# Optimization experiments

Hardware: AMD Instinct MI355X
Metric: run time of the kernel (lower is better)

Reference implementation:

```python
import jax, jax.numpy as jnp
import numpy as np

B, T, F, U, L = 64, 512, 256, 1024, 3
LN_EPS = 1e-12  # tf.contrib.layers.layer_norm default


def setup_inputs() -> dict:
    key = jax.random.key(0)
    ks = jax.random.split(key, 8)

    def w(k, shape):
        return jax.random.normal(k, shape, jnp.float32) / np.float32(np.sqrt(shape[0]))

    return {
        "input": jax.random.normal(ks[0], (B, T, F), jnp.float32),
        "conditioned_lst": jax.random.randint(ks[1], (T,), 0, 2).astype(bool),
        # LSTM layer 0: input = feature F, layers 1..2: input = U
        "W0": w(ks[2], (F + U, 4 * U)), "b0": jnp.zeros((4 * U,), jnp.float32),
        "W1": w(ks[3], (2 * U, 4 * U)), "b1": jnp.zeros((4 * U,), jnp.float32),
        "W2": w(ks[4], (2 * U, 4 * U)), "b2": jnp.zeros((4 * U,), jnp.float32),
        # output dense projection back to feature dim
        "Wd": w(ks[5], (U, F)), "bd": jnp.zeros((F,), jnp.float32),
        # layer norm params
        "gamma": jnp.ones((F,), jnp.float32), "beta": jnp.zeros((F,), jnp.float32),
    }


def _lstm_cell(x, h, c, W, b):
    # BasicLSTMCell: gates in (i, j, f, o) order, forget_bias = 1.0
    z = jnp.dot(jnp.concatenate([x, h], axis=-1), W) + b
    i, j, f, o = jnp.split(z, 4, axis=-1)
    c_new = c * jax.nn.sigmoid(f + 1.0) + jax.nn.sigmoid(i) * jnp.tanh(j)
    h_new = jax.nn.sigmoid(o) * jnp.tanh(c_new)
    return h_new, c_new


def reference(input, conditioned_lst, W0, b0, W1, b1, W2, b2, Wd, bd, gamma, beta):
    Ws, bs = [W0, W1, W2], [b0, b1, b2]
    xs = (jnp.arange(T), jnp.swapaxes(input, 0, 1), conditioned_lst)  # time-major
    carry0 = (jnp.zeros((L, B, U), input.dtype),  # h per layer
              jnp.zeros((L, B, U), input.dtype),  # c per layer
              jnp.zeros((B, F), input.dtype))     # previous emit

    def step(carry, xt):
        hs, cs, prev_emit = carry
        t, x_t, cond_t = xt
        # auto-conditioning: teacher-force on conditioned steps (and step 0)
        x = jnp.where(jnp.logical_or(t == 0, cond_t), x_t, prev_emit)
        new_h, new_c = [], []
        for l in range(L):
            h, c = _lstm_cell(x, hs[l], cs[l], Ws[l], bs[l])
            new_h.append(h)
            new_c.append(c)
            x = h
        y = jnp.dot(x, Wd) + bd  # dense projection [B, F]
        mu = jnp.mean(y, axis=-1, keepdims=True)
        var = jnp.mean(jnp.square(y - mu), axis=-1, keepdims=True)
        y = (y - mu) * jax.lax.rsqrt(var + LN_EPS) * gamma + beta
        emit = jax.nn.relu(y)
        return (jnp.stack(new_h), jnp.stack(new_c), emit), emit

    _, outs = jax.lax.scan(step, carry0, xs)  # [T, B, F]
    return jnp.swapaxes(outs, 0, 1)  # [B, T, F]
```

## Files before the change

kernel.cpp:

```cpp
#include <hip/hip_runtime.h>
#include <math.h>

#define B 64
#define T 512
#define F 256
#define U 1024
#define NBLK 256
#define NTH 512
#define WPAD 68

typedef unsigned short ushort_t;
typedef __attribute__((ext_vector_type(8))) _Float16 f16x8_t;
typedef __attribute__((ext_vector_type(4))) float f32x4_t;

static const size_t OFF_STATS= 0;
static const size_t OFF_COND = 4096;
static const size_t OFF_BAR  = 6144;
static const size_t OFF_H2B  = 7424;
static const size_t OFF_HS   = 269568;
static const size_t OFF_YB   = 1056000;
static const size_t OFF_PW0  = 1088768;
static const size_t OFF_PW1  = 11574528;
static const size_t OFF_PW2  = 28351744;
static const size_t ZERO_BYTES = OFF_PW0;

__device__ __forceinline__ float sigm(float x) {
    return 1.0f / (1.0f + __expf(-x));
}

__device__ __forceinline__ ushort_t f2h(float x) {
    _Float16 h = (_Float16)x;
    union { _Float16 h; ushort_t u; } v; v.h = h;
    return v.u;
}
__device__ __forceinline__ float h2f(ushort_t u) {
    union { ushort_t u; _Float16 h; } v; v.u = u;
    return (float)v.h;
}

__device__ __forceinline__ void store_uc_b64(void* p, unsigned long long v) {
    asm volatile("global_store_dwordx2 %0, %1, off sc0 sc1"
                 :: "v"(p), "v"(v) : "memory");
}
__device__ __forceinline__ void store_uc_b128(void* p, f32x4_t v) {
    asm volatile("global_store_dwordx4 %0, %1, off sc0 sc1"
                 :: "v"(p), "v"(v) : "memory");
}
__device__ __forceinline__ void drain_vmem() {
    asm volatile("s_waitcnt vmcnt(0)" ::: "memory");
}

__device__ __forceinline__ void phase_sync(int* bar, int epoch, int g) {
    drain_vmem();
    __syncthreads();
    if (threadIdx.x == 0) {
        const int sub = g & 7;
        const int prev = __hip_atomic_fetch_add(bar + sub * 16, 1,
                                                __ATOMIC_RELAXED, __HIP_MEMORY_SCOPE_AGENT);
        if (prev == epoch * 32 - 1) {
            const int pm = __hip_atomic_fetch_add(bar + 128, 1,
                                                  __ATOMIC_RELAXED, __HIP_MEMORY_SCOPE_AGENT);
            if (pm == epoch * 8 - 1) {
                #pragma unroll
                for (int i = 0; i < 8; ++i)
                    __hip_atomic_store(bar + 144 + i * 16, epoch, __ATOMIC_RELAXED,
                                       __HIP_MEMORY_SCOPE_AGENT);
            }
        }
        int* myrelay = bar + 144 + sub * 16;
        int spins = 0;
        while (__hip_atomic_load(myrelay, __ATOMIC_RELAXED,
                                 __HIP_MEMORY_SCOPE_AGENT) < epoch) {
            __builtin_amdgcn_s_sleep(1);
            if ((++spins & 255) == 0)
                (void)__hip_atomic_load(myrelay, __ATOMIC_ACQUIRE,
                                        __HIP_MEMORY_SCOPE_AGENT);
        }
    }
    __syncthreads();
}

__global__ void prep_kernel(const unsigned char* __restrict__ condraw,
                            unsigned char* __restrict__ wsb) {
    __shared__ int s_not_int32;
    const int tid = threadIdx.x;
    if (tid == 0) s_not_int32 = 0;
    __syncthreads();
    if (tid < 512 && (tid & 3) != 0) {
        if (condraw[tid] != 0) s_not_int32 = 1;
    }
    __syncthreads();
    const int is32 = (s_not_int32 == 0);
    int* condw = (int*)(wsb + OFF_COND);
    if (tid < 512) {
        int cv = is32 ? ((const int*)condraw)[tid] : (int)condraw[tid];
        condw[tid] = (cv != 0) ? 1 : 0;
    }
}

__global__ void repack_kernel(const float* __restrict__ W0,
                              const float* __restrict__ W1,
                              const float* __restrict__ W2,
                              unsigned char* __restrict__ wsb) {
    ushort_t* P0 = (ushort_t*)(wsb + OFF_PW0);
    ushort_t* P1 = (ushort_t*)(wsb + OFF_PW1);
    ushort_t* P2 = (ushort_t*)(wsb + OFF_PW2);
    const size_t stride = (size_t)gridDim.x * blockDim.x;
    const size_t tid = (size_t)blockIdx.x * blockDim.x + threadIdx.x;
    const size_t N0 = (size_t)256 * 40 * 512;
    const size_t N12 = (size_t)256 * 64 * 512;
    for (size_t i = tid; i < N0; i += stride) {
        const int g = (int)(i / 20480);
        const int r = (int)(i % 20480);
        const int kt = r >> 9, s = r & 511, L = s >> 3, j = s & 7;
        const int k = kt * 32 + ((L >> 4) << 3) + j;
        const int n = L & 15;
        const int col = ((n >> 2) << 10) + (g << 2) + (n & 3);
        P0[i] = f2h(W0[(size_t)k * 4096 + col]);
    }
    for (size_t i = tid; i < N12; i += stride) {
        const int g = (int)(i / 32768);
        const int r = (int)(i % 32768);
        const int kt = r >> 9, s = r & 511, L = s >> 3, j = s & 7;
        const int k = kt * 32 + ((L >> 4) << 3) + j;
        const int n = L & 15;
        const int col = ((n >> 2) << 10) + (g << 2) + (n & 3);
        const size_t src = (size_t)k * 4096 + col;
        P1[i] = f2h(W1[src]);
        P2[i] = f2h(W2[src]);
    }
}

__global__ void __launch_bounds__(NTH, 2)
lstm_persistent(const float* __restrict__ input,
                const float* __restrict__ b0, const float* __restrict__ b1,
                const float* __restrict__ b2,
                const float* __restrict__ Wd, const float* __restrict__ bd,
                const float* __restrict__ gamma, const float* __restrict__ beta,
                float* __restrict__ out, unsigned char* __restrict__ wsb) {
    const int g = blockIdx.x;
    const int tid = threadIdx.x;
    const int lane = tid & 63;
    const int wv = __builtin_amdgcn_readfirstlane(tid >> 6);
    const int ln15 = lane & 15;
    const int quad = lane >> 4;

    float* h2b = (float*)(wsb + OFF_H2B);
    float* stats = (float*)(wsb + OFF_STATS);
    int* bar = (int*)(wsb + OFF_BAR);
    ushort_t* hs = (ushort_t*)(wsb + OFF_HS);
    ushort_t* yb = (ushort_t*)(wsb + OFF_YB);
    const size_t HSZ = (size_t)256 * 64 * 4;

    __shared__ f16x8_t lds_pw0[40 * 64];
    __shared__ f32x4_t lds_wd4[1024];
    __shared__ float zbuf[128 * WPAD];
    __shared__ float zbuf2[128];
    __shared__ float hbuf[64 * 5];
    __shared__ int lds_cond[512];

    const int u0 = g << 2;
    const int f0 = g << 2;
    const int k0 = (wv << 5) + (quad << 3);
    const int fb0 = k0 >> 2;

    f16x8_t Bw1[8], Bw2[8];
    {
        const ushort_t* p1 = (const ushort_t*)(wsb + OFF_PW1) +
                             (size_t)g * 64 * 512 + (size_t)lane * 8;
        const ushort_t* p2 = (const ushort_t*)(wsb + OFF_PW2) +
                             (size_t)g * 64 * 512 + (size_t)lane * 8;
        #pragma unroll
        for (int i = 0; i < 4; ++i) {
            Bw1[i]     = *(const f16x8_t*)(p1 + (size_t)((wv << 2) + i) * 512);
            Bw1[4 + i] = *(const f16x8_t*)(p1 + (size_t)(32 + (wv << 2) + i) * 512);
            Bw2[i]     = *(const f16x8_t*)(p2 + (size_t)((wv << 2) + i) * 512);
            Bw2[4 + i] = *(const f16x8_t*)(p2 + (size_t)(32 + (wv << 2) + i) * 512);
        }
    }
    {
        const f16x8_t* src = (const f16x8_t*)((const ushort_t*)(wsb + OFF_PW0) +
                                              (size_t)g * 40 * 512);
        for (int i = tid; i < 40 * 64; i += NTH) lds_pw0[i] = src[i];
    }
    if (g < 64) {
        for (int k = tid; k < 1024; k += NTH)
            lds_wd4[k] = *(const f32x4_t*)(Wd + (size_t)k * F + f0);
    }
    for (int i = tid; i < 512; i += NTH) lds_cond[i] = ((const int*)(wsb + OFF_COND))[i];

    const int ebo = tid & 63;
    const int euo = (tid >> 6) & 3;

    float bias0[4], bias1[4], bias2[4];
    if (tid < 256) {
        #pragma unroll
        for (int q = 0; q < 4; ++q) {
            bias0[q] = b0[(q << 10) + u0 + euo];
            bias1[q] = b1[(q << 10) + u0 + euo];
            bias2[q] = b2[(q << 10) + u0 + euo];
        }
    }
    float gmv[8], btv[8];
    {
        const float4 g0 = *(const float4*)(gamma + k0);
        const float4 g1 = *(const float4*)(gamma + k0 + 4);
        const float4 t0 = *(const float4*)(beta + k0);
        const float4 t1 = *(const float4*)(beta + k0 + 4);
        gmv[0]=g0.x; gmv[1]=g0.y; gmv[2]=g0.z; gmv[3]=g0.w;
        gmv[4]=g1.x; gmv[5]=g1.y; gmv[6]=g1.z; gmv[7]=g1.w;
        btv[0]=t0.x; btv[1]=t0.y; btv[2]=t0.z; btv[3]=t0.w;
        btv[4]=t1.x; btv[5]=t1.y; btv[6]=t1.z; btv[7]=t1.w;
    }
    float4 gm4 = {0,0,0,0}, bt4 = {0,0,0,0}, bd4 = {0,0,0,0};
    if (g < 64 && wv == 1) {
        gm4 = *(const float4*)(gamma + f0);
        bt4 = *(const float4*)(beta + f0);
    }
    if (g < 64 && wv == 0) {
        bd4 = *(const float4*)(bd + f0);
    }
    __syncthreads();

    float creg0 = 0.f, creg1 = 0.f, creg2 = 0.f;

    f32x4_t acc0[4], acc1[4], acc2[4];
    #pragma unroll
    for (int mt = 0; mt < 4; ++mt) {
        acc0[mt] = (f32x4_t){0.f, 0.f, 0.f, 0.f};
        acc1[mt] = (f32x4_t){0.f, 0.f, 0.f, 0.f};
        acc2[mt] = (f32x4_t){0.f, 0.f, 0.f, 0.f};
    }

    auto ld_frag = [&](const char* p) -> f16x8_t {
        union { unsigned long long q[2]; f16x8_t v; } u;
        u.q[0] = *(const unsigned long long*)(p);
        u.q[1] = *(const unsigned long long*)(p + 512);
        return u.v;
    };

    auto mm4 = [&](f32x4_t (&acc)[4], const ushort_t* base,
                   const f16x8_t (&Bw)[8], const int boff) {
        f16x8_t Ab[4][4];
        const char* bb = (const char*)base + (size_t)ln15 * 8 +
                         (size_t)(quad << 1) * 512;
        #pragma unroll
        for (int c = 0; c < 4; ++c) {
            const char* pc = bb + (size_t)((wv << 2) + c) * 4096;
            #pragma unroll
            for (int mt = 0; mt < 4; ++mt)
                Ab[c][mt] = ld_frag(pc + mt * 128);
        }
        #pragma unroll
        for (int c = 0; c < 4; ++c) {
            #pragma unroll
            for (int mt = 0; mt < 4; ++mt)
                acc[mt] = __builtin_amdgcn_mfma_f32_16x16x32_f16(
                    Ab[c][mt], Bw[boff + c], acc[mt], 0, 0, 0);
        }
    };

    auto mm4_dual_reg = [&](f32x4_t (&accX)[4], const f16x8_t (&BwX)[8],
                            f32x4_t (&accH)[4], const f16x8_t (&BwH)[8],
                            const ushort_t* base) {
        f16x8_t Ab[4][4];
        const char* bb = (const char*)base + (size_t)ln15 * 8 +
                         (size_t)(quad << 1) * 512;
        #pragma unroll
        for (int c = 0; c < 4; ++c) {
            const char* pc = bb + (size_t)((wv << 2) + c) * 4096;
            #pragma unroll
            for (int mt = 0; mt < 4; ++mt)
                Ab[c][mt] = ld_frag(pc + mt * 128);
        }
        #pragma unroll
        for (int c = 0; c < 4; ++c) {
            #pragma unroll
            for (int mt = 0; mt < 4; ++mt)
                accX[mt] = __builtin_amdgcn_mfma_f32_16x16x32_f16(
                    Ab[c][mt], BwX[c], accX[mt], 0, 0, 0);
            #pragma unroll
            for (int mt = 0; mt < 4; ++mt)
                accH[mt] = __builtin_amdgcn_mfma_f32_16x16x32_f16(
                    Ab[c][mt], BwH[4 + c], accH[mt], 0, 0, 0);
        }
    };
    auto mm4_dual_lds0 = [&](f32x4_t (&accX)[4], const f16x8_t (&BwX)[8],
                             f32x4_t (&accH)[4], const ushort_t* base) {
        f16x8_t Ab[4][4];
        const char* bb = (const char*)base + (size_t)ln15 * 8 +
                         (size_t)(quad << 1) * 512;
        #pragma unroll
        for (int c = 0; c < 4; ++c) {
            const char* pc = bb + (size_t)((wv << 2) + c) * 4096;
            #pragma unroll
            for (int mt = 0; mt < 4; ++mt)
                Ab[c][mt] = ld_frag(pc + mt * 128);
        }
        #pragma unroll
        for (int c = 0; c < 4; ++c) {
            const f16x8_t Bh = lds_pw0[(8 + (wv << 2) + c) * 64 + lane];
            #pragma unroll
            for (int mt = 0; mt < 4; ++mt)
                accX[mt] = __builtin_amdgcn_mfma_f32_16x16x32_f16(
                    Ab[c][mt], BwX[c], accX[mt], 0, 0, 0);
            #pragma unroll
            for (int mt = 0; mt < 4; ++mt)
                accH[mt] = __builtin_amdgcn_mfma_f32_16x16x32_f16(
                    Ab[c][mt], Bh, accH[mt], 0, 0, 0);
        }
    };

    auto epilogue = [&](f32x4_t (&acc)[4], const float (&bi)[4], float& cr,
                        ushort_t* hdst, float* h2dst) {
        __syncthreads();
        {
            float* zrow = zbuf + (size_t)(wv * 16 + ln15) * WPAD;
            #pragma unroll
            for (int mt = 0; mt < 4; ++mt)
                *(f32x4_t*)(zrow + mt * 16 + (quad << 2)) = acc[mt];
            #pragma unroll
            for (int mt = 0; mt < 4; ++mt) acc[mt] = (f32x4_t){0.f, 0.f, 0.f, 0.f};
        }
        __syncthreads();
        if (tid < 256) {
            float z[4];
            #pragma unroll
            for (int q = 0; q < 4; ++q) {
                float s = bi[q];
                #pragma unroll
                for (int w = 0; w < 8; ++w)
                    s += zbuf[(size_t)(w * 16 + q * 4 + euo) * WPAD + ebo];
                z[q] = s;
            }
            const float ig = sigm(z[0]);
            const float gg = tanhf(z[1]);
            const float fg = sigm(z[2] + 1.0f);
            const float og = sigm(z[3]);
            const float cn = cr * fg + ig * gg;
            const float hn = og * tanhf(cn);
            cr = cn;
            hbuf[ebo * 5 + euo] = hn;
        }
        __syncthreads();
        if (wv == 0) {
            const float h0v = hbuf[lane * 5 + 0];
            const float h1v = hbuf[lane * 5 + 1];
            const float h2v = hbuf[lane * 5 + 2];
            const float h3v = hbuf[lane * 5 + 3];
            unsigned long long pk =
                (unsigned long long)f2h(h0v) |
                ((unsigned long long)f2h(h1v) << 16) |
                ((unsigned long long)f2h(h2v) << 32) |
                ((unsigned long long)f2h(h3v) << 48);
            store_uc_b64(hdst + (size_t)g * 256 + lane * 4, pk);
        } else if (wv == 1 && h2dst) {
            f32x4_t v;
            v[0] = hbuf[lane * 5 + 0];
            v[1] = hbuf[lane * 5 + 1];
            v[2] = hbuf[lane * 5 + 2];
            v[3] = hbuf[lane * 5 + 3];
            store_uc_b128(h2dst + (size_t)g * 256 + lane * 4, v);
        }
    };

    int epoch = 0;
    for (int t = 0; t < T; ++t) {
        const int p = t & 1;
        const int pn = p ^ 1;
        ushort_t* hs0n = hs + (size_t)(pn * 3 + 0) * HSZ;
        ushort_t* hs1n = hs + (size_t)(pn * 3 + 1) * HSZ;
        ushort_t* hs2n = hs + (size_t)(pn * 3 + 2) * HSZ;

        __builtin_amdgcn_fence(__ATOMIC_ACQUIRE, "agent");

        const int condt = (t == 0) || (lds_cond[t] != 0);
        unsigned long long xr0[4], xr1[4];
        if (condt) {
            #pragma unroll
            for (int mt = 0; mt < 4; ++mt) {
                const int b = ln15 + (mt << 4);
                const float* ip = input + (size_t)b * (T * F) + (size_t)t * F + k0;
                const float4 a0 = *(const float4*)(ip);
                const float4 a1 = *(const float4*)(ip + 4);
                xr0[mt] = (unsigned long long)f2h(a0.x) |
                          ((unsigned long long)f2h(a0.y) << 16) |
                          ((unsigned long long)f2h(a0.z) << 32) |
                          ((unsigned long long)f2h(a0.w) << 48);
                xr1[mt] = (unsigned long long)f2h(a1.x) |
                          ((unsigned long long)f2h(a1.y) << 16) |
                          ((unsigned long long)f2h(a1.z) << 32) |
                          ((unsigned long long)f2h(a1.w) << 48);
            }
        } else {
            #pragma unroll
            for (int mt = 0; mt < 4; ++mt) {
                const int b = ln15 + (mt << 4);
                xr0[mt] = *(const unsigned long long*)(yb + ((size_t)fb0 * 64 + b) * 4);
                xr1[mt] = *(const unsigned long long*)(yb + ((size_t)(fb0 + 1) * 64 + b) * 4);
            }
        }
        unsigned long long yqe = 0;
        if (g < 64 && wv == 1 && t > 0)
            yqe = *(const unsigned long long*)(yb + ((size_t)g * 64 + lane) * 4);
        float2 svst = {0.f, 0.f};
        if (tid < 64)
            svst = *(const float2*)(stats + (size_t)pn * (64 * 8) + tid * 8);
        if (g < 64)
            mm4(acc2, hs + (size_t)(p * 3 + 2) * HSZ, Bw2, 4);
        if (tid < 64) {
            const float mu = svst.x * (1.0f / F);
            const float var = svst.y * (1.0f / F) - mu * mu;
            zbuf2[tid * 2] = mu;
            zbuf2[tid * 2 + 1] = rsqrtf(var + 1e-12f);
        }
        __syncthreads();
        if (g < 64 && wv == 1 && t > 0) {
            union { unsigned long long q; ushort_t s[4]; } yq; yq.q = yqe;
            const float mu = zbuf2[lane * 2], rs = zbuf2[lane * 2 + 1];
            float4 o;
            o.x = fmaxf((h2f(yq.s[0]) - mu) * rs * gm4.x + bt4.x, 0.0f);
            o.y = fmaxf((h2f(yq.s[1]) - mu) * rs * gm4.y + bt4.y, 0.0f);
            o.z = fmaxf((h2f(yq.s[2]) - mu) * rs * gm4.z + bt4.z, 0.0f);
            o.w = fmaxf((h2f(yq.s[3]) - mu) * rs * gm4.w + bt4.w, 0.0f);
            *(float4*)(out + (size_t)lane * (T * F) + (size_t)(t - 1) * F + f0) = o;
        }
        {
            f16x8_t Ax[4];
            #pragma unroll
            for (int mt = 0; mt < 4; ++mt) {
                union { unsigned long long q[2]; f16x8_t v;
                        ushort_t s[8]; } ux;
                if (condt) {
                    ux.q[0] = xr0[mt]; ux.q[1] = xr1[mt];
                } else {
                    const int b = ln15 + (mt << 4);
                    union { unsigned long long q; ushort_t s[4]; } y0, y1;
                    y0.q = xr0[mt]; y1.q = xr1[mt];
                    const float mu = zbuf2[b * 2], rs = zbuf2[b * 2 + 1];
                    #pragma unroll
                    for (int j = 0; j < 4; ++j) {
                        ux.s[j] = f2h(fmaxf((h2f(y0.s[j]) - mu) * rs * gmv[j] + btv[j], 0.0f));
                        ux.s[4 + j] = f2h(fmaxf((h2f(y1.s[j]) - mu) * rs * gmv[4 + j] + btv[4 + j], 0.0f));
                    }
                }
                Ax[mt] = ux.v;
            }
            const f16x8_t Bb = lds_pw0[wv * 64 + lane];
            #pragma unroll
            for (int mt = 0; mt < 4; ++mt)
                acc0[mt] = __builtin_amdgcn_mfma_f32_16x16x32_f16(
                    Ax[mt], Bb, acc0[mt], 0, 0, 0);
        }
        epilogue(acc0, bias0, creg0, hs0n, nullptr);
        phase_sync(bar, ++epoch, g);

        mm4_dual_lds0(acc1, Bw1, acc0, hs0n);
        epilogue(acc1, bias1, creg1, hs1n, nullptr);
        phase_sync(bar, ++epoch, g);

        mm4_dual_reg(acc2, Bw2, acc1, Bw1, hs1n);
        epilogue(acc2, bias2, creg2, hs2n, h2b);
        phase_sync(bar, ++epoch, g);

        if (g < 64) {
            float accd[4] = {0.f, 0.f, 0.f, 0.f};
            #pragma unroll
            for (int half = 0; half < 2; ++half) {
                f32x4_t hv[16];
                const f32x4_t* hb4 = (const f32x4_t*)h2b +
                    (size_t)(wv * 32 + half * 16) * 64 + lane;
                #pragma unroll
                for (int i = 0; i < 16; ++i)
                    hv[i] = hb4[(size_t)i * 64];
                #pragma unroll
                for (int i = 0; i < 16; ++i) {
                    const int k = (wv << 7) + (half << 6) + (i << 2);
                    #pragma unroll
                    for (int j = 0; j < 4; ++j) {
                        const f32x4_t w4 = lds_wd4[k + j];
                        accd[0] = fmaf(w4[0], hv[i][j], accd[0]);
                        accd[1] = fmaf(w4[1], hv[i][j], accd[1]);
                        accd[2] = fmaf(w4[2], hv[i][j], accd[2]);
                        accd[3] = fmaf(w4[3], hv[i][j], accd[3]);
                    }
                }
            }
            __syncthreads();
            #pragma unroll
            for (int jj = 0; jj < 4; ++jj)
                zbuf[(size_t)(wv * 16 + jj) * WPAD + lane] = accd[jj];
            __syncthreads();
            if (wv == 0) {
                float yv[4];
                float s = 0.f, ss = 0.f;
                #pragma unroll
                for (int jj = 0; jj < 4; ++jj) {
                    float y = 0.f;
                    #pragma unroll
                    for (int w = 0; w < 8; ++w)
                        y += zbuf[(size_t)(w * 16 + jj) * WPAD + lane];
                    y += (jj == 0) ? bd4.x : (jj == 1) ? bd4.y : (jj == 2) ? bd4.z : bd4.w;
                    yv[jj] = y;
                    s += y;
                    ss += y * y;
                }
                unsigned long long pk =
                    (unsigned long long)f2h(yv[0]) |
                    ((unsigned long long)f2h(yv[1]) << 16) |
                    ((unsigned long long)f2h(yv[2]) << 32) |
                    ((unsigned long long)f2h(yv[3]) << 48);
                store_uc_b64(yb + ((size_t)g * 64 + lane) * 4, pk);
                float* st = stats + (size_t)p * (64 * 8);
                atomicAdd(&st[(size_t)lane * 8], s);
                atomicAdd(&st[(size_t)lane * 8 + 1], ss);
            }
        } else if (g == 64 && wv == 0) {
            float* st2 = stats + (size_t)pn * (64 * 8);
            store_uc_b64(&st2[(size_t)lane * 8], 0ULL);
        }
        if (g >= 64 && t + 1 < T)
            mm4(acc2, hs2n, Bw2, 4);
        phase_sync(bar, ++epoch, g);
    }

    if (g < 64) {
        __builtin_amdgcn_fence(__ATOMIC_ACQUIRE, "agent");
        if (tid < 64) {
            const float2 sv = *(const float2*)(stats + (size_t)((T - 1) & 1) * (64 * 8) + tid * 8);
            const float mu = sv.x * (1.0f / F);
            const float var = sv.y * (1.0f / F) - mu * mu;
            zbuf2[tid * 2] = mu;
            zbuf2[tid * 2 + 1] = rsqrtf(var + 1e-12f);
        }
        __syncthreads();
        if (wv == 1) {
            union { unsigned long long q; ushort_t s[4]; } yq;
            yq.q = *(const unsigned long long*)(yb + ((size_t)g * 64 + lane) * 4);
            const float mu = zbuf2[lane * 2], rs = zbuf2[lane * 2 + 1];
            float4 o;
            o.x = fmaxf((h2f(yq.s[0]) - mu) * rs * gm4.x + bt4.x, 0.0f);
            o.y = fmaxf((h2f(yq.s[1]) - mu) * rs * gm4.y + bt4.y, 0.0f);
            o.z = fmaxf((h2f(yq.s[2]) - mu) * rs * gm4.z + bt4.z, 0.0f);
            o.w = fmaxf((h2f(yq.s[3]) - mu) * rs * gm4.w + bt4.w, 0.0f);
            *(float4*)(out + (size_t)lane * (T * F) + (size_t)(T - 1) * F + f0) = o;
        }
    }
}

extern "C" void kernel_launch(void* const* d_in, const int* in_sizes, int n_in,
                              void* d_out, int out_size, void* d_ws, size_t ws_size,
                              hipStream_t stream) {
    const float* input = (const float*)d_in[0];
    const unsigned char* condraw = (const unsigned char*)d_in[1];
    const float* W0 = (const float*)d_in[2];
    const float* b0 = (const float*)d_in[3];
    const float* W1 = (const float*)d_in[4];
    const float* b1 = (const float*)d_in[5];
    const float* W2 = (const float*)d_in[6];
    const float* b2 = (const float*)d_in[7];
    const float* Wd = (const float*)d_in[8];
    const float* bd = (const float*)d_in[9];
    const float* gamma = (const float*)d_in[10];
    const float* beta = (const float*)d_in[11];
    float* out = (float*)d_out;
    unsigned char* wsb = (unsigned char*)d_ws;

    hipMemsetAsync(d_ws, 0, ZERO_BYTES, stream);
    prep_kernel<<<1, 512, 0, stream>>>(condraw, wsb);
    repack_kernel<<<2048, 256, 0, stream>>>(W0, W1, W2, wsb);
    lstm_persistent<<<NBLK, NTH, 0, stream>>>(input, b0, b1, b2, Wd, bd,
                                              gamma, beta, out, wsb);
}
```

Measured before the change: 24.12 ms.

## Replace grid barriers after layers 0 and 1 with per-block readiness flags

Drops the full grid-wide phase barriers that followed the layer-0 and layer-1 epilogues. Each block now publishes a per-step flag after its uncached h store, and each wavefront polls only the 32 producer flags whose h slices it reads. This is meant to cut barrier latency and let blocks start the next layer as soon as their inputs are ready. It relies on the ordering of uncached stores and on the flag-to-consumer mapping being correct, and many wavefronts polling flags adds memory traffic.

```diff
diff --git a/kernel.cpp b/kernel.cpp
--- a/kernel.cpp
+++ b/kernel.cpp
@@ -22,6 +22,7 @@
 static const size_t OFF_PW0  = 1088768;
 static const size_t OFF_PW1  = 11574528;
 static const size_t OFF_PW2  = 28351744;
+static const size_t OFF_FLAG = 45128960;
 static const size_t ZERO_BYTES = OFF_PW0;
 
 __device__ __forceinline__ float sigm(float x) {
@@ -38,6 +39,10 @@
     return (float)v.h;
 }
 
+__device__ __forceinline__ void store_uc_u32(int* p, int v) {
+    asm volatile("global_store_dword %0, %1, off sc0 sc1"
+                 :: "v"(p), "v"(v) : "memory");
+}
 __device__ __forceinline__ void store_uc_b64(void* p, unsigned long long v) {
     asm volatile("global_store_dwordx2 %0, %1, off sc0 sc1"
                  :: "v"(p), "v"(v) : "memory");
@@ -78,6 +83,18 @@
         }
     }
     __syncthreads();
+}
+
+__device__ __forceinline__ void wait_flag32(const int* fp, int val, int lane) {
+    for (;;) {
+        int v;
+        asm volatile("global_load_dword %0, %1, off sc0 sc1\n\t"
+                     "s_waitcnt vmcnt(0)"
+                     : "=v"(v) : "v"(fp + (lane & 31)) : "memory");
+        if (__all(v >= val)) break;
+        __builtin_amdgcn_s_sleep(2);
+    }
+    __builtin_amdgcn_sched_barrier(0);
 }
 
 __global__ void prep_kernel(const unsigned char* __restrict__ condraw,
@@ -150,6 +167,8 @@
     int* bar = (int*)(wsb + OFF_BAR);
     ushort_t* hs = (ushort_t*)(wsb + OFF_HS);
     ushort_t* yb = (ushort_t*)(wsb + OFF_YB);
+    int* flags0 = (int*)(wsb + OFF_FLAG);
+    int* flags1 = (int*)(wsb + OFF_FLAG) + 256;
     const size_t HSZ = (size_t)256 * 64 * 4;
 
     __shared__ f16x8_t lds_pw0[40 * 64];
@@ -312,7 +331,7 @@
     };
 
     auto epilogue = [&](f32x4_t (&acc)[4], const float (&bi)[4], float& cr,
-                        ushort_t* hdst, float* h2dst) {
+                        ushort_t* hdst, float* h2dst, int* flagp, int fval) {
         __syncthreads();
         {
             float* zrow = zbuf + (size_t)(wv * 16 + ln15) * WPAD;
@@ -354,6 +373,10 @@
                 ((unsigned long long)f2h(h2v) << 32) |
                 ((unsigned long long)f2h(h3v) << 48);
             store_uc_b64(hdst + (size_t)g * 256 + lane * 4, pk);
+            if (flagp) {
+                drain_vmem();
+                if (lane == 0) store_uc_u32(flagp + g, fval);
+            }
         } else if (wv == 1 && h2dst) {
             f32x4_t v;
             v[0] = hbuf[lane * 5 + 0];
@@ -452,15 +475,15 @@
                 acc0[mt] = __builtin_amdgcn_mfma_f32_16x16x32_f16(
                     Ax[mt], Bb, acc0[mt], 0, 0, 0);
         }
-        epilogue(acc0, bias0, creg0, hs0n, nullptr);
-        phase_sync(bar, ++epoch, g);
-
+        epilogue(acc0, bias0, creg0, hs0n, nullptr, flags0, t + 1);
+
+        wait_flag32(flags0 + 32 * wv, t + 1, lane);
         mm4_dual_lds0(acc1, Bw1, acc0, hs0n);
-        epilogue(acc1, bias1, creg1, hs1n, nullptr);
-        phase_sync(bar, ++epoch, g);
-
+        epilogue(acc1, bias1, creg1, hs1n, nullptr, flags1, t + 1);
+
+        wait_flag32(flags1 + 32 * wv, t + 1, lane);
         mm4_dual_reg(acc2, Bw2, acc1, Bw1, hs1n);
-        epilogue(acc2, bias2, creg2, hs2n, h2b);
+        epilogue(acc2, bias2, creg2, hs2n, h2b, nullptr, 0);
         phase_sync(bar, ++epoch, g);
 
         if (g < 64) {
@@ -567,6 +590,7 @@
     unsigned char* wsb = (unsigned char*)d_ws;
 
     hipMemsetAsync(d_ws, 0, ZERO_BYTES, stream);
+    hipMemsetAsync(wsb + OFF_FLAG, 0, 2048, stream);
     prep_kernel<<<1, 512, 0, stream>>>(condraw, wsb);
     repack_kernel<<<2048, 256, 0, stream>>>(W0, W1, W2, wsb);
     lstm_persistent<<<NBLK, NTH, 0, stream>>>(input, b0, b1, b2, Wd, bd,
```

New measurement: 27.43 ms. 13.7% more time.
